# Performance work log

Measured on AMD Instinct MI355X. Metric: run time of the kernel, lower is better.

The kernel has to match this reference:

```python
import jax, jax.numpy as jnp
import numpy as np

D_IN = 256
D_OUT = 256
N0, N1, N2 = 200000, 40000, 8000
E1, E2 = 1000000, 200000


def setup_inputs() -> dict:
    key = jax.random.key(0)
    ks = jax.random.split(key, 12)
    s = 1.0 / np.sqrt(D_IN)
    nodes = jax.random.normal(ks[0], (N0, D_IN), dtype=jnp.float32)
    W_l1 = jax.random.normal(ks[1], (D_OUT, D_IN), dtype=jnp.float32) * s
    b1 = jnp.zeros((D_OUT,), dtype=jnp.float32)
    W_r1 = jax.random.normal(ks[2], (D_OUT, D_IN), dtype=jnp.float32) * s
    W_l2 = jax.random.normal(ks[3], (D_OUT, D_OUT), dtype=jnp.float32) * s
    b2 = jnp.zeros((D_OUT,), dtype=jnp.float32)
    W_r2 = jax.random.normal(ks[4], (D_OUT, D_OUT), dtype=jnp.float32) * s
    src1 = jax.random.randint(ks[5], (E1,), 0, N0, dtype=jnp.int32)
    dst1 = jax.random.randint(ks[6], (E1,), 0, N1, dtype=jnp.int32)
    src2 = jax.random.randint(ks[7], (E2,), 0, N1, dtype=jnp.int32)
    dst2 = jax.random.randint(ks[8], (E2,), 0, N2, dtype=jnp.int32)
    return {"nodes": nodes, "W_l1": W_l1, "b1": b1, "W_r1": W_r1,
            "W_l2": W_l2, "b2": b2, "W_r2": W_r2,
            "src1": src1, "dst1": dst1, "src2": src2, "dst2": dst2,
            "n1": N1, "n2": N2}


def _sage_layer(x, src, dst, n_tgt, Wl, b, Wr):
    # PyG SAGEConv (mean aggr, bipartite): lin_l(mean_j x_src[j]) + lin_r(x_tgt)
    x_tgt = x[:n_tgt]
    agg = jax.ops.segment_sum(x[src], dst, num_segments=n_tgt)  # [n_tgt, d]
    cnt = jax.ops.segment_sum(jnp.ones(src.shape, dtype=x.dtype), dst,
                              num_segments=n_tgt)
    mean = agg / jnp.maximum(cnt, 1.0)[:, None]
    out = mean @ Wl.T + b + x_tgt @ Wr.T
    return jnp.tanh(out)  # tanh applied by _GraphSAGE.forward


def reference(nodes, W_l1, b1, W_r1, W_l2, b2, W_r2, src1, dst1, src2, dst2, n1, n2):
    h = _sage_layer(nodes, src1, dst1, n1, W_l1, b1, W_r1)  # [n1, D_OUT]
    h = _sage_layer(h, src2, dst2, n2, W_l2, b2, W_r2)      # [n2, D_OUT]
    return h
```

## Files before the change

### kernel.cpp

```cpp
#include <hip/hip_runtime.h>
#include <math.h>

#define D 256
#define KK 512
#define NC1 40
#define NC2 8

typedef __attribute__((ext_vector_type(8))) short short8;
typedef __attribute__((ext_vector_type(4))) float f32x4;

__device__ __forceinline__ unsigned short f2bf(float f) {
    unsigned u = __builtin_bit_cast(unsigned, f);
    u += 0x7fffu + ((u >> 16) & 1u);
    return (unsigned short)(u >> 16);
}
__device__ __forceinline__ float bf2f(unsigned short h) {
    unsigned u = ((unsigned)h) << 16;
    return __builtin_bit_cast(float, u);
}
__device__ __forceinline__ float tanh_fast(float x) {
    return 1.0f - 2.0f / (__expf(2.0f * x) + 1.0f);
}

__global__ __launch_bounds__(256) void prologue(const float* __restrict__ nodes,
                                                unsigned short* __restrict__ nodes_bf, int total8, int CB,
                                                const int* __restrict__ dst1, int E1,
                                                const int* __restrict__ dst2, int E2,
                                                int* cnt1, int* cnt2, int HB,
                                                const float* __restrict__ Wl1, const float* __restrict__ Wr1,
                                                const float* __restrict__ Wl2, const float* __restrict__ Wr2,
                                                unsigned short* Wc1, unsigned short* Wc2) {
    int b = blockIdx.x;
    if (b < CB) {
        int t = b * 256 + threadIdx.x;
        if (t < total8) {
            const float* xp = nodes + (size_t)t * 8;
            float4 v0 = *(const float4*)xp;
            float4 v1 = *(const float4*)(xp + 4);
            unsigned short o[8];
            o[0] = f2bf(v0.x); o[1] = f2bf(v0.y); o[2] = f2bf(v0.z); o[3] = f2bf(v0.w);
            o[4] = f2bf(v1.x); o[5] = f2bf(v1.y); o[6] = f2bf(v1.z); o[7] = f2bf(v1.w);
            *(short8*)(nodes_bf + (size_t)t * 8) = *(short8*)o;
        }
    } else if (b < CB + HB) {
        int t = (b - CB) * 256 + threadIdx.x;
        if (t < E1) {
            atomicAdd(&cnt1[dst1[t]], 1);
        } else if (t < E1 + E2) {
            atomicAdd(&cnt2[dst2[t - E1]], 1);
        }
    } else {
        int t = (b - CB - HB) * 256 + threadIdx.x;
        int which = t >> 17;
        int u = t & 131071;
        int nrow = u >> 9;
        int k = u & 511;
        const float* Wl = which ? Wl2 : Wl1;
        const float* Wr = which ? Wr2 : Wr1;
        unsigned short* Wc = which ? Wc2 : Wc1;
        float v = (k < 256) ? Wl[nrow * 256 + k] : Wr[nrow * 256 + (k - 256)];
        Wc[u] = f2bf(v);
    }
}

__global__ __launch_bounds__(256) void scan_phase1(const int* __restrict__ cnt1, int n1, int* off1, int* part1,
                                                   const int* __restrict__ cnt2, int n2, int* off2, int* part2) {
    int b = blockIdx.x;
    const int* cnt; int n; int* off; int* part; int c;
    if (b < NC1) { cnt = cnt1; n = n1; off = off1; part = part1; c = b; }
    else         { cnt = cnt2; n = n2; off = off2; part = part2; c = b - NC1; }
    int t = threadIdx.x;
    int i0 = c * 1024 + t * 4;
    int v[4];
#pragma unroll
    for (int j = 0; j < 4; ++j) v[j] = (i0 + j < n) ? cnt[i0 + j] : 0;
    int s = v[0] + v[1] + v[2] + v[3];
    int lane = t & 63, wid = t >> 6;
    int ps = s;
#pragma unroll
    for (int d = 1; d < 64; d <<= 1) {
        int tmp = __shfl_up(ps, d);
        if (lane >= d) ps += tmp;
    }
    __shared__ int wsum[4];
    if (lane == 63) wsum[wid] = ps;
    __syncthreads();
    int wbase = 0;
    for (int k = 0; k < wid; ++k) wbase += wsum[k];
    int run = wbase + ps - s;
#pragma unroll
    for (int j = 0; j < 4; ++j) {
        if (i0 + j < n) off[i0 + j] = run;
        run += v[j];
    }
    if (t == 255) part[c] = wbase + ps;
}

__global__ __launch_bounds__(64) void scan_phase2(int* part1, int* part2) {
    if (threadIdx.x == 0) {
        int s = 0;
        for (int i = 0; i < NC1; ++i) { int v = part1[i]; part1[i] = s; s += v; }
        part1[NC1] = s;
    } else if (threadIdx.x == 1) {
        int s = 0;
        for (int i = 0; i < NC2; ++i) { int v = part2[i]; part2[i] = s; s += v; }
        part2[NC2] = s;
    }
}

__global__ __launch_bounds__(256) void scan_phase3_prep(int* off1, const int* __restrict__ cnt1,
                                                        int* cur1, float* recip1, int n1, const int* __restrict__ part1,
                                                        int* off2, const int* __restrict__ cnt2,
                                                        int* cur2, float* recip2, int n2, const int* __restrict__ part2) {
    int b = blockIdx.x;
    int n; int* off; const int* part; const int* cnt; int* cur; float* recip; int c;
    if (b < NC1) { n = n1; off = off1; part = part1; cnt = cnt1; cur = cur1; recip = recip1; c = b; }
    else         { n = n2; off = off2; part = part2; cnt = cnt2; cur = cur2; recip = recip2; c = b - NC1; }
    int t = threadIdx.x;
    int i0 = c * 1024 + t * 4;
    int add = part[c];
#pragma unroll
    for (int j = 0; j < 4; ++j) {
        int i = i0 + j;
        if (i < n) {
            int v = off[i] + add;
            off[i] = v;
            cur[i] = v;
            recip[i] = 1.0f / fmaxf((float)cnt[i], 1.0f);
        }
    }
    if (b == 0 && t == 0) off1[n1] = part1[NC1];
    if (b == NC1 && t == 0) off2[n2] = part2[NC2];
}

__global__ __launch_bounds__(256) void sort_kernel(const int* __restrict__ src1, const int* __restrict__ dst1, int E1,
                                                   int* cur1, int* sorted1,
                                                   const int* __restrict__ src2, const int* __restrict__ dst2, int E2,
                                                   int* cur2, int* sorted2) {
    int t = blockIdx.x * 256 + threadIdx.x;
    if (t < E1) {
        int d = dst1[t];
        int p = atomicAdd(&cur1[d], 1);
        sorted1[p] = src1[t];
    } else if (t < E1 + E2) {
        int u = t - E1;
        int d = dst2[u];
        int p = atomicAdd(&cur2[d], 1);
        sorted2[p] = src2[u];
    }
}

__global__ __launch_bounds__(256) void aggregate_f32(const float* __restrict__ x,
                                                     const int* __restrict__ sorted,
                                                     const int* __restrict__ off,
                                                     const float* __restrict__ recip,
                                                     unsigned short* __restrict__ mean, int n) {
    int node = blockIdx.x * 4 + (threadIdx.x >> 6);
    if (node >= n) return;
    int l = threadIdx.x & 63;
    int beg = off[node], end = off[node + 1];

    float4 a0 = {0.f, 0.f, 0.f, 0.f};
    float4 a1 = {0.f, 0.f, 0.f, 0.f};
    int e = beg;
    for (; e + 1 < end; e += 2) {
        int s0 = sorted[e];
        int s1 = sorted[e + 1];
        float4 v0 = *(const float4*)(x + (size_t)s0 * D + l * 4);
        float4 v1 = *(const float4*)(x + (size_t)s1 * D + l * 4);
        a0.x += v0.x; a0.y += v0.y; a0.z += v0.z; a0.w += v0.w;
        a1.x += v1.x; a1.y += v1.y; a1.z += v1.z; a1.w += v1.w;
    }
    if (e < end) {
        int s = sorted[e];
        float4 v = *(const float4*)(x + (size_t)s * D + l * 4);
        a0.x += v.x; a0.y += v.y; a0.z += v.z; a0.w += v.w;
    }
    float r = recip[node];
    ushort4 o;
    o.x = f2bf((a0.x + a1.x) * r);
    o.y = f2bf((a0.y + a1.y) * r);
    o.z = f2bf((a0.z + a1.z) * r);
    o.w = f2bf((a0.w + a1.w) * r);
    *(ushort4*)(mean + (size_t)node * D + l * 4) = o;
}

__global__ __launch_bounds__(256) void aggregate_bf16(const unsigned short* __restrict__ x,
                                                      const int* __restrict__ sorted,
                                                      const int* __restrict__ off,
                                                      const float* __restrict__ recip,
                                                      unsigned short* __restrict__ mean, int n) {
    int node = blockIdx.x * 4 + (threadIdx.x >> 6);
    if (node >= n) return;
    int l = threadIdx.x & 63;
    int slot = l >> 5;
    int li = l & 31;
    int beg = off[node], end = off[node + 1];

    float a0[8] = {}, a1[8] = {}, a2[8] = {}, a3[8] = {};
    int e = beg;
    for (; e + 7 < end; e += 8) {
        int s0 = sorted[e + slot];
        int s1 = sorted[e + 2 + slot];
        int s2 = sorted[e + 4 + slot];
        int s3 = sorted[e + 6 + slot];
        short8 v0 = *(const short8*)(x + (size_t)s0 * D + li * 8);
        short8 v1 = *(const short8*)(x + (size_t)s1 * D + li * 8);
        short8 v2 = *(const short8*)(x + (size_t)s2 * D + li * 8);
        short8 v3 = *(const short8*)(x + (size_t)s3 * D + li * 8);
#pragma unroll
        for (int k = 0; k < 8; ++k) {
            a0[k] += bf2f((unsigned short)v0[k]);
            a1[k] += bf2f((unsigned short)v1[k]);
            a2[k] += bf2f((unsigned short)v2[k]);
            a3[k] += bf2f((unsigned short)v3[k]);
        }
    }
    for (; e < end; e += 2) {
        int me = e + slot;
        if (me < end) {
            int s = sorted[me];
            short8 v = *(const short8*)(x + (size_t)s * D + li * 8);
#pragma unroll
            for (int k = 0; k < 8; ++k) a0[k] += bf2f((unsigned short)v[k]);
        }
    }
    float r = recip[node];
    unsigned short o[8];
#pragma unroll
    for (int k = 0; k < 8; ++k) {
        float t = a0[k] + a1[k] + a2[k] + a3[k];
        t += __shfl_xor(t, 32);
        o[k] = f2bf(t * r);
    }
    if (slot == 0)
        *(short8*)(mean + (size_t)node * D + li * 8) = *(short8*)o;
}

template<bool X_FP32, bool OUT_BF16>
__global__ __launch_bounds__(256) void sage_gemm_mfma(const unsigned short* __restrict__ meanp,
                                                      const void* __restrict__ xp,
                                                      const unsigned short* __restrict__ Wcat,
                                                      const float* __restrict__ bias,
                                                      void* __restrict__ outp,
                                                      int M) {
    __shared__ unsigned short Asb[128 * 72];
    __shared__ unsigned short Wsb[128 * 72];

    const int tid = threadIdx.x;
    const int lane = tid & 63;
    const int w = tid >> 6;
    const int wm = w & 1, wn = w >> 1;
    const int quad = lane >> 4, lr = lane & 15;
    const int row0 = blockIdx.x * 128;
    const int n0 = blockIdx.y * 128;

    f32x4 acc[4][4] = {};

    for (int kt = 0; kt < 8; ++kt) {
        const bool mh = (kt < 4);
        const int kg0 = mh ? kt * 64 : (kt - 4) * 64;

#pragma unroll
        for (int i = 0; i < 4; ++i) {
            int f = i * 256 + tid;
            int r = f >> 3;
            int c8 = (f & 7) * 8;
            int gr = row0 + r;
            unsigned short tmp[8];
            if (gr < M) {
                if (mh) {
                    *(short8*)tmp = *(const short8*)(meanp + (size_t)gr * D + kg0 + c8);
                } else if (X_FP32) {
                    const float* xf = (const float*)xp + (size_t)gr * D + kg0 + c8;
                    float4 v0 = *(const float4*)xf;
                    float4 v1 = *(const float4*)(xf + 4);
                    tmp[0] = f2bf(v0.x); tmp[1] = f2bf(v0.y); tmp[2] = f2bf(v0.z); tmp[3] = f2bf(v0.w);
                    tmp[4] = f2bf(v1.x); tmp[5] = f2bf(v1.y); tmp[6] = f2bf(v1.z); tmp[7] = f2bf(v1.w);
                } else {
                    *(short8*)tmp = *(const short8*)((const unsigned short*)xp + (size_t)gr * D + kg0 + c8);
                }
            } else {
#pragma unroll
                for (int j = 0; j < 8; ++j) tmp[j] = 0;
            }
            *(short8*)&Asb[r * 72 + c8] = *(short8*)tmp;
        }

#pragma unroll
        for (int i = 0; i < 4; ++i) {
            int f = i * 256 + tid;
            int nn = f >> 3;
            int c8 = (f & 7) * 8;
            *(short8*)&Wsb[nn * 72 + c8] =
                *(const short8*)(Wcat + (size_t)(n0 + nn) * KK + kt * 64 + c8);
        }

        __syncthreads();

#pragma unroll
        for (int ks = 0; ks < 64; ks += 32) {
            short8 a[4], b[4];
#pragma unroll
            for (int mt = 0; mt < 4; ++mt)
                a[mt] = *(const short8*)&Asb[(wm * 64 + mt * 16 + lr) * 72 + ks + quad * 8];
#pragma unroll
            for (int nt = 0; nt < 4; ++nt)
                b[nt] = *(const short8*)&Wsb[(wn * 64 + nt * 16 + lr) * 72 + ks + quad * 8];
#pragma unroll
            for (int mt = 0; mt < 4; ++mt)
#pragma unroll
                for (int nt = 0; nt < 4; ++nt)
                    acc[mt][nt] = __builtin_amdgcn_mfma_f32_16x16x32_bf16(a[mt], b[nt], acc[mt][nt], 0, 0, 0);
        }

        __syncthreads();
    }

#pragma unroll
    for (int mt = 0; mt < 4; ++mt) {
        int gr0 = row0 + wm * 64 + mt * 16 + quad * 4;
#pragma unroll
        for (int nt = 0; nt < 4; ++nt) {
            int col = n0 + wn * 64 + nt * 16 + lr;
            float bc = bias[col];
#pragma unroll
            for (int r = 0; r < 4; ++r) {
                int gr = gr0 + r;
                if (gr < M) {
                    float v = tanh_fast(acc[mt][nt][r] + bc);
                    if (OUT_BF16) ((unsigned short*)outp)[(size_t)gr * D + col] = f2bf(v);
                    else          ((float*)outp)[(size_t)gr * D + col] = v;
                }
            }
        }
    }
}

extern "C" void kernel_launch(void* const* d_in, const int* in_sizes, int n_in,
                              void* d_out, int out_size, void* d_ws, size_t ws_size,
                              hipStream_t stream) {
    const float* nodes = (const float*)d_in[0];
    const float* W_l1  = (const float*)d_in[1];
    const float* b1    = (const float*)d_in[2];
    const float* W_r1  = (const float*)d_in[3];
    const float* W_l2  = (const float*)d_in[4];
    const float* b2    = (const float*)d_in[5];
    const float* W_r2  = (const float*)d_in[6];
    const int* src1 = (const int*)d_in[7];
    const int* dst1 = (const int*)d_in[8];
    const int* src2 = (const int*)d_in[9];
    const int* dst2 = (const int*)d_in[10];

    const int E1 = in_sizes[7];
    const int E2 = in_sizes[9];
    const int N0 = in_sizes[0] / D;
    const int N1 = 40000;
    const int N2 = 8000;

    char* p = (char*)d_ws;
    auto carve = [&](size_t bytes) -> char* {
        char* q = p;
        p += (bytes + 255) & ~(size_t)255;
        return q;
    };
    unsigned short* mean1 = (unsigned short*)carve((size_t)N1 * D * 2);
    unsigned short* h1    = (unsigned short*)carve((size_t)N1 * D * 2);
    unsigned short* mean2 = (unsigned short*)carve((size_t)N2 * D * 2);
    unsigned short* Wc1   = (unsigned short*)carve((size_t)D * KK * 2);
    unsigned short* Wc2   = (unsigned short*)carve((size_t)D * KK * 2);
    float* recip1 = (float*)carve((size_t)N1 * 4);
    float* recip2 = (float*)carve((size_t)N2 * 4);
    int* cnt1 = (int*)carve((size_t)(N1 + N2) * 4);
    int* cnt2 = cnt1 + N1;
    int* off1 = (int*)carve((size_t)(N1 + 1) * 4);
    int* off2 = (int*)carve((size_t)(N2 + 1) * 4);
    int* cur1 = (int*)carve((size_t)N1 * 4);
    int* cur2 = (int*)carve((size_t)N2 * 4);
    int* part1 = (int*)carve((size_t)(NC1 + 1) * 4);
    int* part2 = (int*)carve((size_t)(NC2 + 1) * 4);
    int* sorted1 = (int*)carve((size_t)E1 * 4);
    int* sorted2 = (int*)carve((size_t)E2 * 4);
    unsigned short* nodes_bf = (unsigned short*)carve((size_t)N0 * D * 2);
    const bool use_bf = ((size_t)(p - (char*)d_ws) <= ws_size);

    hipMemsetAsync(cnt1, 0, (size_t)(N1 + N2) * sizeof(int), stream);

    const int totE = E1 + E2;
    const int total8 = N0 * D / 8;
    const int CB = use_bf ? (total8 + 255) / 256 : 0;
    const int HB = (totE + 255) / 256;
    const int WB = (2 * D * KK + 255) / 256;

    prologue<<<CB + HB + WB, 256, 0, stream>>>(nodes, nodes_bf, total8, CB,
                                               dst1, E1, dst2, E2, cnt1, cnt2, HB,
                                               W_l1, W_r1, W_l2, W_r2, Wc1, Wc2);
    scan_phase1<<<NC1 + NC2, 256, 0, stream>>>(cnt1, N1, off1, part1, cnt2, N2, off2, part2);
    scan_phase2<<<1, 64, 0, stream>>>(part1, part2);
    scan_phase3_prep<<<NC1 + NC2, 256, 0, stream>>>(off1, cnt1, cur1, recip1, N1, part1,
                                                    off2, cnt2, cur2, recip2, N2, part2);
    sort_kernel<<<(totE + 255) / 256, 256, 0, stream>>>(src1, dst1, E1, cur1, sorted1,
                                                        src2, dst2, E2, cur2, sorted2);

    if (use_bf) {
        aggregate_bf16<<<N1 / 4, 256, 0, stream>>>(nodes_bf, sorted1, off1, recip1, mean1, N1);
        sage_gemm_mfma<false, true><<<dim3((N1 + 127) / 128, 2), 256, 0, stream>>>(
            mean1, (const void*)nodes_bf, Wc1, b1, (void*)h1, N1);
    } else {
        aggregate_f32<<<N1 / 4, 256, 0, stream>>>(nodes, sorted1, off1, recip1, mean1, N1);
        sage_gemm_mfma<true, true><<<dim3((N1 + 127) / 128, 2), 256, 0, stream>>>(
            mean1, (const void*)nodes, Wc1, b1, (void*)h1, N1);
    }

    aggregate_bf16<<<N2 / 4, 256, 0, stream>>>(h1, sorted2, off2, recip2, mean2, N2);
    sage_gemm_mfma<false, false><<<dim3((N2 + 127) / 128, 2), 256, 0, stream>>>(
        mean2, (const void*)h1, Wc2, b2, d_out, N2);
}
```

Baseline: 598.3 us.

## Drop full bf16 conversion of nodes; gather fp32 directly with deeper unroll

Measured after the change: 621.1 us. +3.8%, slower.

```diff
diff --git a/kernel.cpp b/kernel.cpp
--- a/kernel.cpp
+++ b/kernel.cpp
@@ -22,35 +22,22 @@
     return 1.0f - 2.0f / (__expf(2.0f * x) + 1.0f);
 }
 
-__global__ __launch_bounds__(256) void prologue(const float* __restrict__ nodes,
-                                                unsigned short* __restrict__ nodes_bf, int total8, int CB,
-                                                const int* __restrict__ dst1, int E1,
-                                                const int* __restrict__ dst2, int E2,
-                                                int* cnt1, int* cnt2, int HB,
-                                                const float* __restrict__ Wl1, const float* __restrict__ Wr1,
-                                                const float* __restrict__ Wl2, const float* __restrict__ Wr2,
-                                                unsigned short* Wc1, unsigned short* Wc2) {
+__global__ __launch_bounds__(256) void hw_kernel(const int* __restrict__ dst1, int E1,
+                                                 const int* __restrict__ dst2, int E2,
+                                                 int* cnt1, int* cnt2, int HB,
+                                                 const float* __restrict__ Wl1, const float* __restrict__ Wr1,
+                                                 const float* __restrict__ Wl2, const float* __restrict__ Wr2,
+                                                 unsigned short* Wc1, unsigned short* Wc2) {
     int b = blockIdx.x;
-    if (b < CB) {
+    if (b < HB) {
         int t = b * 256 + threadIdx.x;
-        if (t < total8) {
-            const float* xp = nodes + (size_t)t * 8;
-            float4 v0 = *(const float4*)xp;
-            float4 v1 = *(const float4*)(xp + 4);
-            unsigned short o[8];
-            o[0] = f2bf(v0.x); o[1] = f2bf(v0.y); o[2] = f2bf(v0.z); o[3] = f2bf(v0.w);
-            o[4] = f2bf(v1.x); o[5] = f2bf(v1.y); o[6] = f2bf(v1.z); o[7] = f2bf(v1.w);
-            *(short8*)(nodes_bf + (size_t)t * 8) = *(short8*)o;
-        }
-    } else if (b < CB + HB) {
-        int t = (b - CB) * 256 + threadIdx.x;
         if (t < E1) {
             atomicAdd(&cnt1[dst1[t]], 1);
         } else if (t < E1 + E2) {
             atomicAdd(&cnt2[dst2[t - E1]], 1);
         }
     } else {
-        int t = (b - CB - HB) * 256 + threadIdx.x;
+        int t = (b - HB) * 256 + threadIdx.x;
         int which = t >> 17;
         int u = t & 131071;
         int nrow = u >> 9;
@@ -150,38 +137,42 @@
     }
 }
 
-__global__ __launch_bounds__(256) void aggregate_f32(const float* __restrict__ x,
-                                                     const int* __restrict__ sorted,
-                                                     const int* __restrict__ off,
-                                                     const float* __restrict__ recip,
-                                                     unsigned short* __restrict__ mean, int n) {
+__global__ __launch_bounds__(256) void aggregate_f32v(const float* __restrict__ x,
+                                                      const int* __restrict__ sorted,
+                                                      const int* __restrict__ off,
+                                                      const float* __restrict__ recip,
+                                                      unsigned short* __restrict__ mean, int n) {
     int node = blockIdx.x * 4 + (threadIdx.x >> 6);
     if (node >= n) return;
     int l = threadIdx.x & 63;
     int beg = off[node], end = off[node + 1];
 
-    float4 a0 = {0.f, 0.f, 0.f, 0.f};
-    float4 a1 = {0.f, 0.f, 0.f, 0.f};
+    float4 a0 = {0.f,0.f,0.f,0.f}, a1 = {0.f,0.f,0.f,0.f};
+    float4 a2 = {0.f,0.f,0.f,0.f}, a3 = {0.f,0.f,0.f,0.f};
     int e = beg;
-    for (; e + 1 < end; e += 2) {
-        int s0 = sorted[e];
-        int s1 = sorted[e + 1];
-        float4 v0 = *(const float4*)(x + (size_t)s0 * D + l * 4);
-        float4 v1 = *(const float4*)(x + (size_t)s1 * D + l * 4);
-        a0.x += v0.x; a0.y += v0.y; a0.z += v0.z; a0.w += v0.w;
-        a1.x += v1.x; a1.y += v1.y; a1.z += v1.z; a1.w += v1.w;
-    }
-    if (e < end) {
+    for (; e + 7 < end; e += 8) {
+        int s[8];
+#pragma unroll
+        for (int j = 0; j < 8; ++j) s[j] = sorted[e + j];
+        float4 t[8];
+#pragma unroll
+        for (int j = 0; j < 8; ++j) t[j] = *(const float4*)(x + (size_t)s[j] * D + l * 4);
+        a0.x += t[0].x + t[4].x; a0.y += t[0].y + t[4].y; a0.z += t[0].z + t[4].z; a0.w += t[0].w + t[4].w;
+        a1.x += t[1].x + t[5].x; a1.y += t[1].y + t[5].y; a1.z += t[1].z + t[5].z; a1.w += t[1].w + t[5].w;
+        a2.x += t[2].x + t[6].x; a2.y += t[2].y + t[6].y; a2.z += t[2].z + t[6].z; a2.w += t[2].w + t[6].w;
+        a3.x += t[3].x + t[7].x; a3.y += t[3].y + t[7].y; a3.z += t[3].z + t[7].z; a3.w += t[3].w + t[7].w;
+    }
+    for (; e < end; ++e) {
         int s = sorted[e];
         float4 v = *(const float4*)(x + (size_t)s * D + l * 4);
         a0.x += v.x; a0.y += v.y; a0.z += v.z; a0.w += v.w;
     }
     float r = recip[node];
     ushort4 o;
-    o.x = f2bf((a0.x + a1.x) * r);
-    o.y = f2bf((a0.y + a1.y) * r);
-    o.z = f2bf((a0.z + a1.z) * r);
-    o.w = f2bf((a0.w + a1.w) * r);
+    o.x = f2bf((a0.x + a1.x + a2.x + a3.x) * r);
+    o.y = f2bf((a0.y + a1.y + a2.y + a3.y) * r);
+    o.z = f2bf((a0.z + a1.z + a2.z + a3.z) * r);
+    o.w = f2bf((a0.w + a1.w + a2.w + a3.w) * r);
     *(ushort4*)(mean + (size_t)node * D + l * 4) = o;
 }
 
@@ -354,7 +345,6 @@
 
     const int E1 = in_sizes[7];
     const int E2 = in_sizes[9];
-    const int N0 = in_sizes[0] / D;
     const int N1 = 40000;
     const int N2 = 8000;
 
@@ -381,20 +371,15 @@
     int* part2 = (int*)carve((size_t)(NC2 + 1) * 4);
     int* sorted1 = (int*)carve((size_t)E1 * 4);
     int* sorted2 = (int*)carve((size_t)E2 * 4);
-    unsigned short* nodes_bf = (unsigned short*)carve((size_t)N0 * D * 2);
-    const bool use_bf = ((size_t)(p - (char*)d_ws) <= ws_size);
 
     hipMemsetAsync(cnt1, 0, (size_t)(N1 + N2) * sizeof(int), stream);
 
     const int totE = E1 + E2;
-    const int total8 = N0 * D / 8;
-    const int CB = use_bf ? (total8 + 255) / 256 : 0;
     const int HB = (totE + 255) / 256;
     const int WB = (2 * D * KK + 255) / 256;
 
-    prologue<<<CB + HB + WB, 256, 0, stream>>>(nodes, nodes_bf, total8, CB,
-                                               dst1, E1, dst2, E2, cnt1, cnt2, HB,
-                                               W_l1, W_r1, W_l2, W_r2, Wc1, Wc2);
+    hw_kernel<<<HB + WB, 256, 0, stream>>>(dst1, E1, dst2, E2, cnt1, cnt2, HB,
+                                           W_l1, W_r1, W_l2, W_r2, Wc1, Wc2);
     scan_phase1<<<NC1 + NC2, 256, 0, stream>>>(cnt1, N1, off1, part1, cnt2, N2, off2, part2);
     scan_phase2<<<1, 64, 0, stream>>>(part1, part2);
     scan_phase3_prep<<<NC1 + NC2, 256, 0, stream>>>(off1, cnt1, cur1, recip1, N1, part1,
@@ -402,15 +387,9 @@
     sort_kernel<<<(totE + 255) / 256, 256, 0, stream>>>(src1, dst1, E1, cur1, sorted1,
                                                         src2, dst2, E2, cur2, sorted2);
 
-    if (use_bf) {
-        aggregate_bf16<<<N1 / 4, 256, 0, stream>>>(nodes_bf, sorted1, off1, recip1, mean1, N1);
-        sage_gemm_mfma<false, true><<<dim3((N1 + 127) / 128, 2), 256, 0, stream>>>(
-            mean1, (const void*)nodes_bf, Wc1, b1, (void*)h1, N1);
-    } else {
-        aggregate_f32<<<N1 / 4, 256, 0, stream>>>(nodes, sorted1, off1, recip1, mean1, N1);
-        sage_gemm_mfma<true, true><<<dim3((N1 + 127) / 128, 2), 256, 0, stream>>>(
-            mean1, (const void*)nodes, Wc1, b1, (void*)h1, N1);
-    }
+    aggregate_f32v<<<N1 / 4, 256, 0, stream>>>(nodes, sorted1, off1, recip1, mean1, N1);
+    sage_gemm_mfma<true, true><<<dim3((N1 + 127) / 128, 2), 256, 0, stream>>>(
+        mean1, (const void*)nodes, Wc1, b1, (void*)h1, N1);
 
     aggregate_bf16<<<N2 / 4, 256, 0, stream>>>(h1, sorted2, off2, recip2, mean2, N2);
     sage_gemm_mfma<false, false><<<dim3((N2 + 127) / 128, 2), 256, 0, stream>>>(
```
